# Optimization experiments

Hardware: AMD Instinct MI355X
Metric: run time of the kernel (lower is better)

## Reference

```python
import jax, jax.numpy as jnp
import numpy as np

NC = 80        # number of classes
CONF = 0.25    # confidence threshold
RATIO = 0.1    # top-k fraction


def setup_inputs() -> dict:
    key = jax.random.key(0)
    N = 2097152
    data = jax.random.normal(key, (1, N, 4 + NC), dtype=jnp.float32)
    return {"data": data}


def reference(data):
    pred = data[0]                      # [N, 4+nc]
    cls_logits = pred[:, -NC:]          # [N, nc]
    boxes = pred[:, :4]                 # [N, 4]
    scores = jnp.max(cls_logits, axis=1)  # class_id is None -> max over classes
    n = scores.shape[0]
    k = max(1, min(n, int(np.ceil(n * float(RATIO)))))  # static k
    vals, idx = jax.lax.top_k(scores, k)   # [k], [k]
    mask = vals >= CONF                     # [k] bool
    # torch returns 0.0 when mask is empty; masked sums naturally give 0 then.
    loss = jnp.sum(jnp.where(mask, vals, 0.0))
    # output_type == 'all' -> add gathered box sums for masked top-k indices
    loss = loss + jnp.sum(jnp.where(mask[:, None], boxes[idx], 0.0))
    return loss
```

## Files before the change

### kernel.cpp

```cpp
#include <hip/hip_runtime.h>
#include <stdint.h>
#include <math.h>

#define ROWLEN 84
#define F4PR 21
#define RPB 128
#define F4PT (RPB * F4PR)
#define CANDCAP (1u << 21)

__device__ __forceinline__ uint32_t map_f(float f) {
    uint32_t u = __float_as_uint(f);
    return (u & 0x80000000u) ? ~u : (u | 0x80000000u);
}
__device__ __forceinline__ float unmap_f(uint32_t u) {
    uint32_t b = (u & 0x80000000u) ? (u & 0x7FFFFFFFu) : ~u;
    return __uint_as_float(b);
}

__device__ void find_parallel(const uint32_t* hist, int nbins, uint32_t target,
                              uint32_t* s, uint32_t* sc2, uint32_t* outBin, uint32_t* outAbove) {
    int tid = threadIdx.x;
    int chunks = nbins / 256;
    int base = tid * chunks;
    uint32_t part = 0;
    for (int i = 0; i < chunks; ++i) part += hist[base + i];
    s[tid] = part;
    __syncthreads();
    for (int off = 1; off < 256; off <<= 1) {
        uint32_t v = (tid + off < 256) ? s[tid + off] : 0u;
        __syncthreads();
        s[tid] += v;
        __syncthreads();
    }
    uint32_t above_next = (tid < 255) ? s[tid + 1] : 0u;
    bool mine = (s[tid] >= target) && (above_next < target);
    if (mine) { sc2[0] = (uint32_t)tid; sc2[1] = above_next; }
    __syncthreads();
    uint32_t c = sc2[0], above = sc2[1];
    if (tid == 0) {
        uint32_t acc = above;
        int b = (int)c * chunks + chunks - 1;
        for (;; --b) {
            uint32_t hb = hist[b];
            if (acc + hb >= target) break;
            acc += hb;
        }
        sc2[0] = (uint32_t)b;
        sc2[1] = acc;
    }
    __syncthreads();
    *outBin = sc2[0];
    *outAbove = sc2[1];
}

__global__ __launch_bounds__(256) void k_score_hist(const float* __restrict__ pred,
                                                    uint32_t* __restrict__ scores,
                                                    uint32_t* __restrict__ gH1,
                                                    float* __restrict__ out, int n) {
    __shared__ float pm[F4PT];
    __shared__ uint32_t h[1024];
    int tid = threadIdx.x;
    if (blockIdx.x == 0 && tid == 0) *out = 0.f;
    for (int i = tid; i < 1024; i += 256) h[i] = 0;
    uint32_t tid21 = (uint32_t)tid % 21u;
    const float4* pf4 = (const float4*)pred;
    size_t total_f4 = (size_t)n * F4PR;
    int ntiles = (n + RPB - 1) / RPB;
    int lane = tid & 63;
    int rloc = (tid >> 6) * 32 + (lane >> 1);
    int par = lane & 1;
    for (int tile = blockIdx.x; tile < ntiles; tile += gridDim.x) {
        __syncthreads();
        size_t gbase = (size_t)tile * F4PT;
        int row0 = tile * RPB;
        if (row0 + RPB <= n) {
#pragma unroll
            for (int it = 0; it < 11; ++it) {
                int l = it * 256 + tid;
                if (l < F4PT) {
                    const uint32_t BP = (21u - (4u * (uint32_t)it) % 21u) % 21u;
                    float4 v = pf4[gbase + l];
                    float m = fmaxf(fmaxf(v.x, v.y), fmaxf(v.z, v.w));
                    pm[l] = (tid21 == BP) ? -INFINITY : m;
                }
            }
        } else {
#pragma unroll
            for (int it = 0; it < 11; ++it) {
                int l = it * 256 + tid;
                if (l < F4PT) {
                    const uint32_t BP = (21u - (4u * (uint32_t)it) % 21u) % 21u;
                    size_t g = gbase + l;
                    float m = -INFINITY;
                    if (g < total_f4 && tid21 != BP) {
                        float4 v = pf4[g];
                        m = fmaxf(fmaxf(v.x, v.y), fmaxf(v.z, v.w));
                    }
                    pm[l] = m;
                }
            }
        }
        __syncthreads();
        const float* q = pm + rloc * F4PR + 1 + par * 10;
        float m = q[0];
#pragma unroll
        for (int j = 1; j < 10; ++j) m = fmaxf(m, q[j]);
        m = fmaxf(m, __shfl_xor(m, 1));
        int row = row0 + rloc;
        if (par == 0 && row < n) {
            uint32_t u = map_f(m);
            scores[row] = u;
            atomicAdd(&h[u >> 22], 1u);
        }
    }
    __syncthreads();
    for (int i = tid; i < 1024; i += 256)
        if (h[i]) atomicAdd(&gH1[i], h[i]);
}

__global__ void k_hist2f(const uint32_t* __restrict__ scores, const uint32_t* __restrict__ gH1,
                         uint32_t* __restrict__ gH2, uint32_t* __restrict__ sres,
                         int n, uint32_t K) {
    __shared__ uint32_t h[2048];
    __shared__ uint32_t s[256];
    __shared__ uint32_t sc2[2];
    for (int i = threadIdx.x; i < 2048; i += 256) h[i] = 0;
    uint32_t bin1, chi1;
    find_parallel(gH1, 1024, K, s, sc2, &bin1, &chi1);
    if (blockIdx.x == 0 && threadIdx.x == 0) { sres[0] = bin1; sres[1] = chi1; }
    int gid = blockIdx.x * 256 + threadIdx.x;
    int stride = gridDim.x * 256;
    const uint4* s4 = (const uint4*)scores;
    int n4 = n >> 2;
    for (int i = gid; i < n4; i += stride) {
        uint4 uu = s4[i];
        if ((uu.x >> 22) == bin1) atomicAdd(&h[(uu.x >> 11) & 0x7FFu], 1u);
        if ((uu.y >> 22) == bin1) atomicAdd(&h[(uu.y >> 11) & 0x7FFu], 1u);
        if ((uu.z >> 22) == bin1) atomicAdd(&h[(uu.z >> 11) & 0x7FFu], 1u);
        if ((uu.w >> 22) == bin1) atomicAdd(&h[(uu.w >> 11) & 0x7FFu], 1u);
    }
    for (int r = n4 * 4 + gid; r < n; r += stride) {
        uint32_t u = scores[r];
        if ((u >> 22) == bin1) atomicAdd(&h[(u >> 11) & 0x7FFu], 1u);
    }
    __syncthreads();
    for (int i = threadIdx.x; i < 2048; i += 256)
        if (h[i]) atomicAdd(&gH2[i], h[i]);
}

__global__ void k_select2(const float* __restrict__ pred, const uint32_t* __restrict__ scores,
                          const uint32_t* __restrict__ gH2, const uint32_t* __restrict__ sres,
                          uint32_t* __restrict__ candCnt, unsigned long long* __restrict__ candBuf,
                          uint32_t* __restrict__ done, float* __restrict__ out,
                          int n, uint32_t K) {
    __shared__ uint32_t h[2048];
    __shared__ uint32_t s[256];
    __shared__ uint32_t sc2[2];
    __shared__ float wsum[4];
    __shared__ uint32_t tb[1024];
    __shared__ uint32_t tc;
    __shared__ uint32_t s_last;
    int tid = threadIdx.x;
    uint32_t bin1 = sres[0], chi1 = sres[1];
    uint32_t bin2, chi2;
    find_parallel(gH2, 2048, K - chi1, s, sc2, &bin2, &chi2);
    uint32_t t21 = (bin1 << 11) | bin2;
    uint32_t chiTot = chi1 + chi2;
    uint32_t mprime = K - chiTot;
    const uint32_t u_conf = 0xBE800000u;
    const uint32_t CONF21 = u_conf >> 11;
    bool tcut = (t21 >= CONF21);
    float lsum = 0.f;
    int gid = blockIdx.x * 256 + tid;
    int stride = gridDim.x * 256;
    const uint4* s4 = (const uint4*)scores;
    int n4 = n >> 2;
    for (int i = gid; i < n4; i += stride) {
        uint4 uu = s4[i];
#pragma unroll
        for (int j = 0; j < 4; ++j) {
            uint32_t u = (j == 0) ? uu.x : (j == 1) ? uu.y : (j == 2) ? uu.z : uu.w;
            int r = i * 4 + j;
            bool sel = tcut ? ((u >> 11) > t21) : (u >= u_conf);
            if (sel) {
                float4 b = *(const float4*)(pred + (size_t)r * ROWLEN);
                lsum += unmap_f(u) + b.x + b.y + b.z + b.w;
            }
            if (tcut && (u >> 11) == t21) {
                uint32_t pos = atomicAdd(candCnt, 1u);
                if (pos < CANDCAP) {
                    unsigned long long v = ((unsigned long long)u << 32) | (uint32_t)r;
                    __hip_atomic_store(&candBuf[pos], v, __ATOMIC_RELAXED,
                                       __HIP_MEMORY_SCOPE_AGENT);
                }
            }
        }
    }
    for (int r = n4 * 4 + gid; r < n; r += stride) {
        uint32_t u = scores[r];
        bool sel = tcut ? ((u >> 11) > t21) : (u >= u_conf);
        if (sel) {
            float4 b = *(const float4*)(pred + (size_t)r * ROWLEN);
            lsum += unmap_f(u) + b.x + b.y + b.z + b.w;
        }
        if (tcut && (u >> 11) == t21) {
            uint32_t pos = atomicAdd(candCnt, 1u);
            if (pos < CANDCAP) {
                unsigned long long v = ((unsigned long long)u << 32) | (uint32_t)r;
                __hip_atomic_store(&candBuf[pos], v, __ATOMIC_RELAXED, __HIP_MEMORY_SCOPE_AGENT);
            }
        }
    }
    for (int off = 32; off; off >>= 1) lsum += __shfl_down(lsum, off);
    int wid = tid >> 6, lane = tid & 63;
    if (lane == 0) wsum[wid] = lsum;
    __syncthreads();
    if (tid == 0) {
        atomicAdd(out, wsum[0] + wsum[1] + wsum[2] + wsum[3]);
        uint32_t prev = __hip_atomic_fetch_add(done, 1u, __ATOMIC_ACQ_REL,
                                               __HIP_MEMORY_SCOPE_AGENT);
        s_last = (prev == gridDim.x - 1) ? 1u : 0u;
    }
    __syncthreads();
    if (!s_last || !tcut) return;

    uint32_t cc = __hip_atomic_load(candCnt, __ATOMIC_RELAXED, __HIP_MEMORY_SCOPE_AGENT);
    if (cc > CANDCAP) cc = CANDCAP;
    for (int i = tid; i < 2048; i += 256) h[i] = 0;
    if (tid == 0) tc = 0;
    __syncthreads();
    for (uint32_t i = tid; i < cc; i += 256) {
        unsigned long long v = __hip_atomic_load(&candBuf[i], __ATOMIC_RELAXED,
                                                 __HIP_MEMORY_SCOPE_AGENT);
        atomicAdd(&h[(uint32_t)(v >> 32) & 0x7FFu], 1u);
    }
    __syncthreads();
    uint32_t bin3, chi3;
    find_parallel(h, 2048, mprime, s, sc2, &bin3, &chi3);
    uint32_t t_u = (t21 << 11) | bin3;
    uint32_t mt = mprime - chi3;
    float fsum = 0.f;
    for (uint32_t i = tid; i < cc; i += 256) {
        unsigned long long v = __hip_atomic_load(&candBuf[i], __ATOMIC_RELAXED,
                                                 __HIP_MEMORY_SCOPE_AGENT);
        uint32_t key = (uint32_t)(v >> 32);
        uint32_t r = (uint32_t)v;
        uint32_t low = key & 0x7FFu;
        if (low > bin3) {
            float4 b = *(const float4*)(pred + (size_t)r * ROWLEN);
            fsum += unmap_f(key) + b.x + b.y + b.z + b.w;
        } else if (low == bin3) {
            uint32_t p = atomicAdd(&tc, 1u);
            if (p < 1024) tb[p] = r;
        }
    }
    __syncthreads();
    uint32_t tcnt = tc;
    if (tcnt > 1024) tcnt = 1024;
    if (mt >= tcnt) {
        for (uint32_t i = tid; i < tcnt; i += 256) {
            float4 b = *(const float4*)(pred + (size_t)tb[i] * ROWLEN);
            fsum += b.x + b.y + b.z + b.w;
        }
    } else {
        for (uint32_t i = tid; i < tcnt; i += 256) {
            uint32_t ri = tb[i];
            uint32_t rank = 0;
            for (uint32_t j = 0; j < tcnt; ++j) rank += (tb[j] < ri) ? 1u : 0u;
            if (rank < mt) {
                float4 b = *(const float4*)(pred + (size_t)ri * ROWLEN);
                fsum += b.x + b.y + b.z + b.w;
            }
        }
    }
    for (int off = 32; off; off >>= 1) fsum += __shfl_down(fsum, off);
    if (lane == 0) wsum[wid] = fsum;
    __syncthreads();
    if (tid == 0)
        atomicAdd(out, wsum[0] + wsum[1] + wsum[2] + wsum[3] + (float)mt * unmap_f(t_u));
}

extern "C" void kernel_launch(void* const* d_in, const int* in_sizes, int n_in,
                              void* d_out, int out_size, void* d_ws, size_t ws_size,
                              hipStream_t stream) {
    const float* pred = (const float*)d_in[0];
    int n = in_sizes[0] / ROWLEN;
    double kd = ceil((double)n * 0.1);
    long kk = (long)kd;
    if (kk < 1) kk = 1;
    if (kk > n) kk = n;
    uint32_t K = (uint32_t)kk;

    uint32_t* ws32 = (uint32_t*)d_ws;
    uint32_t* scores = ws32;
    uint32_t* gH1 = ws32 + n;
    uint32_t* gH2 = gH1 + 1024;
    uint32_t* candCnt = gH2 + 2048;
    uint32_t* done = candCnt + 16;
    uint32_t* sres = done + 16;
    unsigned long long* candBuf = (unsigned long long*)(sres + 16);
    float* out = (float*)d_out;

    hipMemsetAsync(gH1, 0, (1024 + 2048 + 16 + 16) * sizeof(uint32_t), stream);

    k_score_hist<<<2048, 256, 0, stream>>>(pred, scores, gH1, out, n);
    k_hist2f<<<1024, 256, 0, stream>>>(scores, gH1, gH2, sres, n, K);
    k_select2<<<2048, 256, 0, stream>>>(pred, scores, gH2, sres, candCnt, candBuf,
                                        done, out, n, K);
}
```

Before: 232.5 us.

## Build full 21-bit global histogram in score pass and drop second histogram kernel

The score kernel now also atomically increments a 2M-bin global histogram indexed by the top 21 bits of each score, so the separate k_hist2f pass that re-read all scores is removed. k_select2 finds both radix bins directly from the global histograms, and the last-block tail is split into a separate single-block k_final kernel instead of a done-counter handshake. Rows per tile double to 256 with one thread computing each row's max serially. In exchange this adds an 8 MB memset and one global atomic per row, which may contend heavily in the dense bins.

```diff
diff --git a/kernel.cpp b/kernel.cpp
--- a/kernel.cpp
+++ b/kernel.cpp
@@ -4,7 +4,7 @@
 
 #define ROWLEN 84
 #define F4PR 21
-#define RPB 128
+#define RPB 256
 #define F4PT (RPB * F4PR)
 #define CANDCAP (1u << 21)
 
@@ -56,6 +56,7 @@
 __global__ __launch_bounds__(256) void k_score_hist(const float* __restrict__ pred,
                                                     uint32_t* __restrict__ scores,
                                                     uint32_t* __restrict__ gH1,
+                                                    uint32_t* __restrict__ gH21,
                                                     float* __restrict__ out, int n) {
     __shared__ float pm[F4PT];
     __shared__ uint32_t h[1024];
@@ -66,51 +67,43 @@
     const float4* pf4 = (const float4*)pred;
     size_t total_f4 = (size_t)n * F4PR;
     int ntiles = (n + RPB - 1) / RPB;
-    int lane = tid & 63;
-    int rloc = (tid >> 6) * 32 + (lane >> 1);
-    int par = lane & 1;
     for (int tile = blockIdx.x; tile < ntiles; tile += gridDim.x) {
         __syncthreads();
         size_t gbase = (size_t)tile * F4PT;
         int row0 = tile * RPB;
         if (row0 + RPB <= n) {
 #pragma unroll
-            for (int it = 0; it < 11; ++it) {
+            for (int it = 0; it < F4PR; ++it) {
+                const uint32_t BP = (21u - (4u * (uint32_t)it) % 21u) % 21u;
+                float4 v = pf4[gbase + it * 256 + tid];
+                float m = fmaxf(fmaxf(v.x, v.y), fmaxf(v.z, v.w));
+                pm[it * 256 + tid] = (tid21 == BP) ? -INFINITY : m;
+            }
+        } else {
+#pragma unroll
+            for (int it = 0; it < F4PR; ++it) {
+                const uint32_t BP = (21u - (4u * (uint32_t)it) % 21u) % 21u;
                 int l = it * 256 + tid;
-                if (l < F4PT) {
-                    const uint32_t BP = (21u - (4u * (uint32_t)it) % 21u) % 21u;
-                    float4 v = pf4[gbase + l];
-                    float m = fmaxf(fmaxf(v.x, v.y), fmaxf(v.z, v.w));
-                    pm[l] = (tid21 == BP) ? -INFINITY : m;
+                size_t g = gbase + l;
+                float m = -INFINITY;
+                if (g < total_f4 && tid21 != BP) {
+                    float4 v = pf4[g];
+                    m = fmaxf(fmaxf(v.x, v.y), fmaxf(v.z, v.w));
                 }
-            }
-        } else {
-#pragma unroll
-            for (int it = 0; it < 11; ++it) {
-                int l = it * 256 + tid;
-                if (l < F4PT) {
-                    const uint32_t BP = (21u - (4u * (uint32_t)it) % 21u) % 21u;
-                    size_t g = gbase + l;
-                    float m = -INFINITY;
-                    if (g < total_f4 && tid21 != BP) {
-                        float4 v = pf4[g];
-                        m = fmaxf(fmaxf(v.x, v.y), fmaxf(v.z, v.w));
-                    }
-                    pm[l] = m;
-                }
-            }
-        }
-        __syncthreads();
-        const float* q = pm + rloc * F4PR + 1 + par * 10;
-        float m = q[0];
-#pragma unroll
-        for (int j = 1; j < 10; ++j) m = fmaxf(m, q[j]);
-        m = fmaxf(m, __shfl_xor(m, 1));
-        int row = row0 + rloc;
-        if (par == 0 && row < n) {
+                pm[l] = m;
+            }
+        }
+        __syncthreads();
+        int row = row0 + tid;
+        if (row < n) {
+            const float* q = pm + tid * F4PR;
+            float m = q[1];
+#pragma unroll
+            for (int j = 2; j <= 20; ++j) m = fmaxf(m, q[j]);
             uint32_t u = map_f(m);
             scores[row] = u;
             atomicAdd(&h[u >> 22], 1u);
+            atomicAdd(&gH21[u >> 11], 1u);
         }
     }
     __syncthreads();
@@ -118,55 +111,23 @@
         if (h[i]) atomicAdd(&gH1[i], h[i]);
 }
 
-__global__ void k_hist2f(const uint32_t* __restrict__ scores, const uint32_t* __restrict__ gH1,
-                         uint32_t* __restrict__ gH2, uint32_t* __restrict__ sres,
-                         int n, uint32_t K) {
-    __shared__ uint32_t h[2048];
-    __shared__ uint32_t s[256];
-    __shared__ uint32_t sc2[2];
-    for (int i = threadIdx.x; i < 2048; i += 256) h[i] = 0;
-    uint32_t bin1, chi1;
-    find_parallel(gH1, 1024, K, s, sc2, &bin1, &chi1);
-    if (blockIdx.x == 0 && threadIdx.x == 0) { sres[0] = bin1; sres[1] = chi1; }
-    int gid = blockIdx.x * 256 + threadIdx.x;
-    int stride = gridDim.x * 256;
-    const uint4* s4 = (const uint4*)scores;
-    int n4 = n >> 2;
-    for (int i = gid; i < n4; i += stride) {
-        uint4 uu = s4[i];
-        if ((uu.x >> 22) == bin1) atomicAdd(&h[(uu.x >> 11) & 0x7FFu], 1u);
-        if ((uu.y >> 22) == bin1) atomicAdd(&h[(uu.y >> 11) & 0x7FFu], 1u);
-        if ((uu.z >> 22) == bin1) atomicAdd(&h[(uu.z >> 11) & 0x7FFu], 1u);
-        if ((uu.w >> 22) == bin1) atomicAdd(&h[(uu.w >> 11) & 0x7FFu], 1u);
-    }
-    for (int r = n4 * 4 + gid; r < n; r += stride) {
-        uint32_t u = scores[r];
-        if ((u >> 22) == bin1) atomicAdd(&h[(u >> 11) & 0x7FFu], 1u);
-    }
-    __syncthreads();
-    for (int i = threadIdx.x; i < 2048; i += 256)
-        if (h[i]) atomicAdd(&gH2[i], h[i]);
-}
-
 __global__ void k_select2(const float* __restrict__ pred, const uint32_t* __restrict__ scores,
-                          const uint32_t* __restrict__ gH2, const uint32_t* __restrict__ sres,
-                          uint32_t* __restrict__ candCnt, unsigned long long* __restrict__ candBuf,
-                          uint32_t* __restrict__ done, float* __restrict__ out,
-                          int n, uint32_t K) {
-    __shared__ uint32_t h[2048];
+                          const uint32_t* __restrict__ gH1, const uint32_t* __restrict__ gH21,
+                          uint32_t* __restrict__ sres, uint32_t* __restrict__ candCnt,
+                          unsigned long long* __restrict__ candBuf,
+                          float* __restrict__ out, int n, uint32_t K) {
     __shared__ uint32_t s[256];
     __shared__ uint32_t sc2[2];
     __shared__ float wsum[4];
-    __shared__ uint32_t tb[1024];
-    __shared__ uint32_t tc;
-    __shared__ uint32_t s_last;
-    int tid = threadIdx.x;
-    uint32_t bin1 = sres[0], chi1 = sres[1];
+    int tid = threadIdx.x;
+    uint32_t bin1, chi1;
+    find_parallel(gH1, 1024, K, s, sc2, &bin1, &chi1);
     uint32_t bin2, chi2;
-    find_parallel(gH2, 2048, K - chi1, s, sc2, &bin2, &chi2);
+    find_parallel(gH21 + ((size_t)bin1 << 11), 2048, K - chi1, s, sc2, &bin2, &chi2);
     uint32_t t21 = (bin1 << 11) | bin2;
     uint32_t chiTot = chi1 + chi2;
     uint32_t mprime = K - chiTot;
+    if (blockIdx.x == 0 && tid == 0) { sres[2] = t21; sres[4] = mprime; }
     const uint32_t u_conf = 0xBE800000u;
     const uint32_t CONF21 = u_conf >> 11;
     bool tcut = (t21 >= CONF21);
@@ -188,11 +149,8 @@
             }
             if (tcut && (u >> 11) == t21) {
                 uint32_t pos = atomicAdd(candCnt, 1u);
-                if (pos < CANDCAP) {
-                    unsigned long long v = ((unsigned long long)u << 32) | (uint32_t)r;
-                    __hip_atomic_store(&candBuf[pos], v, __ATOMIC_RELAXED,
-                                       __HIP_MEMORY_SCOPE_AGENT);
-                }
+                if (pos < CANDCAP)
+                    candBuf[pos] = ((unsigned long long)u << 32) | (uint32_t)r;
             }
         }
     }
@@ -205,35 +163,40 @@
         }
         if (tcut && (u >> 11) == t21) {
             uint32_t pos = atomicAdd(candCnt, 1u);
-            if (pos < CANDCAP) {
-                unsigned long long v = ((unsigned long long)u << 32) | (uint32_t)r;
-                __hip_atomic_store(&candBuf[pos], v, __ATOMIC_RELAXED, __HIP_MEMORY_SCOPE_AGENT);
-            }
+            if (pos < CANDCAP)
+                candBuf[pos] = ((unsigned long long)u << 32) | (uint32_t)r;
         }
     }
     for (int off = 32; off; off >>= 1) lsum += __shfl_down(lsum, off);
     int wid = tid >> 6, lane = tid & 63;
     if (lane == 0) wsum[wid] = lsum;
     __syncthreads();
-    if (tid == 0) {
-        atomicAdd(out, wsum[0] + wsum[1] + wsum[2] + wsum[3]);
-        uint32_t prev = __hip_atomic_fetch_add(done, 1u, __ATOMIC_ACQ_REL,
-                                               __HIP_MEMORY_SCOPE_AGENT);
-        s_last = (prev == gridDim.x - 1) ? 1u : 0u;
-    }
-    __syncthreads();
-    if (!s_last || !tcut) return;
-
-    uint32_t cc = __hip_atomic_load(candCnt, __ATOMIC_RELAXED, __HIP_MEMORY_SCOPE_AGENT);
+    if (tid == 0) atomicAdd(out, wsum[0] + wsum[1] + wsum[2] + wsum[3]);
+}
+
+__global__ void k_final(const float* __restrict__ pred, const uint32_t* __restrict__ sres,
+                        const uint32_t* __restrict__ candCnt,
+                        const unsigned long long* __restrict__ candBuf,
+                        float* __restrict__ out) {
+    __shared__ uint32_t h[2048];
+    __shared__ uint32_t s[256];
+    __shared__ uint32_t sc2[2];
+    __shared__ float wsum[4];
+    __shared__ uint32_t tb[1024];
+    __shared__ uint32_t tc;
+    uint32_t t21 = sres[2];
+    const uint32_t u_conf = 0xBE800000u;
+    const uint32_t CONF21 = u_conf >> 11;
+    if (t21 < CONF21) return;
+    uint32_t mprime = sres[4];
+    uint32_t cc = *candCnt;
     if (cc > CANDCAP) cc = CANDCAP;
+    int tid = threadIdx.x;
     for (int i = tid; i < 2048; i += 256) h[i] = 0;
     if (tid == 0) tc = 0;
     __syncthreads();
-    for (uint32_t i = tid; i < cc; i += 256) {
-        unsigned long long v = __hip_atomic_load(&candBuf[i], __ATOMIC_RELAXED,
-                                                 __HIP_MEMORY_SCOPE_AGENT);
-        atomicAdd(&h[(uint32_t)(v >> 32) & 0x7FFu], 1u);
-    }
+    for (uint32_t i = tid; i < cc; i += 256)
+        atomicAdd(&h[(uint32_t)(candBuf[i] >> 32) & 0x7FFu], 1u);
     __syncthreads();
     uint32_t bin3, chi3;
     find_parallel(h, 2048, mprime, s, sc2, &bin3, &chi3);
@@ -241,8 +204,7 @@
     uint32_t mt = mprime - chi3;
     float fsum = 0.f;
     for (uint32_t i = tid; i < cc; i += 256) {
-        unsigned long long v = __hip_atomic_load(&candBuf[i], __ATOMIC_RELAXED,
-                                                 __HIP_MEMORY_SCOPE_AGENT);
+        unsigned long long v = candBuf[i];
         uint32_t key = (uint32_t)(v >> 32);
         uint32_t r = (uint32_t)v;
         uint32_t low = key & 0x7FFu;
@@ -274,6 +236,7 @@
         }
     }
     for (int off = 32; off; off >>= 1) fsum += __shfl_down(fsum, off);
+    int wid = tid >> 6, lane = tid & 63;
     if (lane == 0) wsum[wid] = fsum;
     __syncthreads();
     if (tid == 0)
@@ -294,17 +257,16 @@
     uint32_t* ws32 = (uint32_t*)d_ws;
     uint32_t* scores = ws32;
     uint32_t* gH1 = ws32 + n;
-    uint32_t* gH2 = gH1 + 1024;
-    uint32_t* candCnt = gH2 + 2048;
-    uint32_t* done = candCnt + 16;
-    uint32_t* sres = done + 16;
-    unsigned long long* candBuf = (unsigned long long*)(sres + 16);
+    uint32_t* candCnt = gH1 + 1024;
+    uint32_t* sres = candCnt + 16;
+    uint32_t* gH21 = sres + 16;
+    unsigned long long* candBuf = (unsigned long long*)(gH21 + (1u << 21));
     float* out = (float*)d_out;
 
-    hipMemsetAsync(gH1, 0, (1024 + 2048 + 16 + 16) * sizeof(uint32_t), stream);
-
-    k_score_hist<<<2048, 256, 0, stream>>>(pred, scores, gH1, out, n);
-    k_hist2f<<<1024, 256, 0, stream>>>(scores, gH1, gH2, sres, n, K);
-    k_select2<<<2048, 256, 0, stream>>>(pred, scores, gH2, sres, candCnt, candBuf,
-                                        done, out, n, K);
-}
+    hipMemsetAsync(gH1, 0, (1024 + 16 + 16 + (1u << 21)) * sizeof(uint32_t), stream);
+
+    k_score_hist<<<2048, 256, 0, stream>>>(pred, scores, gH1, gH21, out, n);
+    k_select2<<<2048, 256, 0, stream>>>(pred, scores, gH1, gH21, sres, candCnt, candBuf,
+                                        out, n, K);
+    k_final<<<1, 256, 0, stream>>>(pred, sres, candCnt, candBuf, out);
+}
```

After: 314.3 us. +35.2%, slower.
